# Optimization experiments

Hardware: AMD Instinct MI355X
Metric: run time of the kernel (lower is better)

Reference implementation:

```python
import jax, jax.numpy as jnp
import numpy as np

H = 16  # num heads
DH = 64  # head dim


def setup_inputs() -> dict:
    key = jax.random.key(0)
    ks = jax.random.split(key, 9)
    d = 1024
    s = 0.02
    return {
        "hidden_states": jax.random.normal(ks[0], (16, 1024, d), jnp.float32),
        "Wq": jax.random.normal(ks[1], (d, d), jnp.float32) * s,
        "bq": jax.random.normal(ks[2], (d,), jnp.float32) * s,
        "Wk": jax.random.normal(ks[3], (d, d), jnp.float32) * s,
        "bk": jax.random.normal(ks[4], (d,), jnp.float32) * s,
        "Wv": jax.random.normal(ks[5], (d, d), jnp.float32) * s,
        "bv": jax.random.normal(ks[6], (d,), jnp.float32) * s,
        "Wo": jax.random.normal(ks[7], (d, d), jnp.float32) * s,
        "bo": jax.random.normal(ks[8], (d,), jnp.float32) * s,
    }


def _heads(x):
    b, s, _ = x.shape
    return x.reshape(b, s, H, DH).transpose(0, 2, 1, 3)  # [B,H,S,Dh]


def reference(hidden_states, Wq, bq, Wk, bk, Wv, bv, Wo, bo):
    # torch nn.Linear: y = x @ W.T + b; weights here are [out, in]
    q = _heads(hidden_states @ Wq.T + bq)
    k = _heads(hidden_states @ Wk.T + bk)
    v = _heads(hidden_states @ Wv.T + bv)
    scores = jnp.einsum("bhqd,bhkd->bhqk", q, k) / jnp.sqrt(jnp.float32(DH))
    probs = jax.nn.softmax(scores, axis=-1)
    ctx = jnp.einsum("bhqk,bhkd->bhqd", probs, v)
    b, _, s, _ = ctx.shape
    ctx = ctx.transpose(0, 2, 1, 3).reshape(b, s, H * DH)
    out = ctx @ Wo.T + bo
    # module returns (attention_output, weights=None); return array only
    return out
```

## Files before the change

kernel.cpp:

```cpp
#include <hip/hip_runtime.h>
#include <hip/hip_bf16.h>
#include <stdint.h>


typedef short bf16x8 __attribute__((ext_vector_type(8)));
typedef float f32x4 __attribute__((ext_vector_type(4)));
typedef unsigned short ushort_t;
typedef ushort_t us8 __attribute__((ext_vector_type(8)));

__device__ __forceinline__ ushort_t f2b(float f) {
    unsigned x;
    __builtin_memcpy(&x, &f, 4);
    unsigned r = (x + 0x7fffu + ((x >> 16) & 1u)) >> 16;
    return (ushort_t)r;
}
__device__ __forceinline__ unsigned fbits(float f) {
    unsigned x;
    __builtin_memcpy(&x, &f, 4);
    return x;
}

__device__ __forceinline__ void glds16(const void* g, void* l) {
    __builtin_amdgcn_global_load_lds(
        (const __attribute__((address_space(1))) void*)g,
        (__attribute__((address_space(3))) void*)l, 16, 0, 0);
}

#define MFMA(a, b, c) __builtin_amdgcn_mfma_f32_16x16x32_bf16((a), (b), (c), 0, 0, 0)

__global__ __launch_bounds__(256, 8) void cvt_f32_bf16_kernel(
    const float* __restrict__ in, ushort_t* __restrict__ out, int n8)
{
    int i = blockIdx.x * 256 + threadIdx.x;
    if (i >= n8) return;
    const float4* p = (const float4*)in + (size_t)i * 2;
    float4 a = p[0], b = p[1];
    us8 v;
    v[0] = f2b(a.x); v[1] = f2b(a.y); v[2] = f2b(a.z); v[3] = f2b(a.w);
    v[4] = f2b(b.x); v[5] = f2b(b.y); v[6] = f2b(b.z); v[7] = f2b(b.w);
    *((us8*)out + i) = v;
}

template <bool OUTF>
__global__ __launch_bounds__(256, 2) void gemm_bias_kernel(
    const ushort_t* __restrict__ A,
    const ushort_t* __restrict__ W0, const ushort_t* __restrict__ W1, const ushort_t* __restrict__ W2,
    const float* __restrict__ b0, const float* __restrict__ b1, const float* __restrict__ b2,
    void* __restrict__ C0, void* __restrict__ C1, void* __restrict__ C2,
    int M, int N, int K)
{
    const ushort_t* W = (blockIdx.z == 0) ? W0 : ((blockIdx.z == 1) ? W1 : W2);
    const float* bias = (blockIdx.z == 0) ? b0 : ((blockIdx.z == 1) ? b1 : b2);
    void* C = (blockIdx.z == 0) ? C0 : ((blockIdx.z == 1) ? C1 : C2);

    __shared__ ushort_t As[128 * 64];
    __shared__ ushort_t Bs[128 * 64];

    const int tid = threadIdx.x;
    const int lane = tid & 63;
    const int wave = tid >> 6;
    const int bm = blockIdx.x * 128;
    const int bn = blockIdx.y * 128;
    const int wm = (wave >> 1) * 64;
    const int wn = (wave & 1) * 64;
    const int q = lane >> 4;
    const int ml = lane & 15;

    f32x4 acc[4][4] = {};

    for (int k0 = 0; k0 < K; k0 += 64) {
        __syncthreads();
#pragma unroll
        for (int it = 0; it < 4; ++it) {
            int cid = it * 256 + tid;
            int r = cid >> 3;
            int s = cid & 7;
            int sc = s ^ (r & 7);
            glds16(A + (size_t)(bm + r) * K + k0 + sc * 8, As + cid * 8);
            glds16(W + (size_t)(bn + r) * K + k0 + sc * 8, Bs + cid * 8);
        }
        __syncthreads();
#pragma unroll
        for (int ks = 0; ks < 2; ++ks) {
            bf16x8 af[4], bfr[4];
#pragma unroll
            for (int i = 0; i < 4; ++i) {
                int row = wm + i * 16 + ml;
                int ch = (ks * 4 + q) ^ (row & 7);
                af[i] = *(const bf16x8*)(As + row * 64 + ch * 8);
                int rowb = wn + i * 16 + ml;
                int chb = (ks * 4 + q) ^ (rowb & 7);
                bfr[i] = *(const bf16x8*)(Bs + rowb * 64 + chb * 8);
            }
#pragma unroll
            for (int i = 0; i < 4; ++i)
#pragma unroll
                for (int j = 0; j < 4; ++j)
                    acc[i][j] = MFMA(af[i], bfr[j], acc[i][j]);
        }
    }

#pragma unroll
    for (int j = 0; j < 4; ++j) {
        int col = bn + wn + j * 16 + ml;
        float bv = bias[col];
#pragma unroll
        for (int i = 0; i < 4; ++i) {
            int rowb = bm + wm + i * 16 + q * 4;
#pragma unroll
            for (int r = 0; r < 4; ++r) {
                float v = acc[i][j][r] + bv;
                if (OUTF)
                    ((float*)C)[(size_t)(rowb + r) * N + col] = v;
                else
                    ((ushort_t*)C)[(size_t)(rowb + r) * N + col] = f2b(v);
            }
        }
    }
}

__global__ __launch_bounds__(256, 4) void transpose_v_kernel(
    const ushort_t* __restrict__ V, ushort_t* __restrict__ Vt)
{
    __shared__ ushort_t t[64 * 65];
    const int bh = blockIdx.x;
    const int st = blockIdx.y;
    const int b = bh >> 4, h = bh & 15;
    const int tid = threadIdx.x;

#pragma unroll
    for (int i = 0; i < 16; ++i) {
        int e = i * 256 + tid;
        int s = e >> 6, d = e & 63;
        t[s * 65 + d] = V[(size_t)(b * 1024 + st * 64 + s) * 1024 + h * 64 + d];
    }
    __syncthreads();
#pragma unroll
    for (int i = 0; i < 16; ++i) {
        int e = i * 256 + tid;
        int d = e >> 6, s = e & 63;
        Vt[(size_t)(bh * 64 + d) * 1024 + st * 64 + s] = t[s * 65 + d];
    }
}

__global__ __launch_bounds__(256, 2) void attn_kernel(
    const ushort_t* __restrict__ Q, const ushort_t* __restrict__ K,
    const ushort_t* __restrict__ Vt, ushort_t* __restrict__ ctx)
{
    __shared__ ushort_t Ks[64 * 64];
    __shared__ ushort_t Vs[64 * 64];
    __shared__ ushort_t Ps[4][32 * 72];

    const int bh = blockIdx.x;
    const int qt = blockIdx.y;
    const int b = bh >> 4, h = bh & 15;
    const int tid = threadIdx.x;
    const int lane = tid & 63;
    const int wave = tid >> 6;
    const int q = lane >> 4;
    const int ml = lane & 15;

    bf16x8 qf[2][2];
#pragma unroll
    for (int mg = 0; mg < 2; ++mg) {
        int row = b * 1024 + qt * 128 + wave * 32 + mg * 16 + ml;
        const ushort_t* qp = Q + (size_t)row * 1024 + h * 64;
        qf[mg][0] = *(const bf16x8*)(qp + q * 8);
        qf[mg][1] = *(const bf16x8*)(qp + 32 + q * 8);
    }

    f32x4 o[2][4] = {};
    float l[2] = {0.f, 0.f};
    const float cexp = 1.4426950408889634f * 0.125f;

    ushort_t* Pw = Ps[wave];

    for (int kt = 0; kt < 16; ++kt) {
        __syncthreads();
#pragma unroll
        for (int it = 0; it < 2; ++it) {
            int cid = it * 256 + tid;
            int r = cid >> 3, s = cid & 7, sc = s ^ (r & 7);
            glds16(K + (size_t)(b * 1024 + kt * 64 + r) * 1024 + h * 64 + sc * 8,
                   Ks + cid * 8);
            glds16(Vt + (size_t)(bh * 64 + r) * 1024 + kt * 64 + sc * 8,
                   Vs + cid * 8);
        }
        __syncthreads();

#pragma unroll
        for (int n = 0; n < 4; ++n) {
            int row = n * 16 + ml;
            int c0 = q ^ (row & 7);
            int c1 = (4 + q) ^ (row & 7);
            bf16x8 k0 = *(const bf16x8*)(Ks + row * 64 + c0 * 8);
            bf16x8 k1 = *(const bf16x8*)(Ks + row * 64 + c1 * 8);
#pragma unroll
            for (int mg = 0; mg < 2; ++mg) {
                f32x4 z = {};
                z = MFMA(k0, qf[mg][0], z);
                z = MFMA(k1, qf[mg][1], z);
                float p0 = exp2f(z[0] * cexp);
                float p1 = exp2f(z[1] * cexp);
                float p2 = exp2f(z[2] * cexp);
                float p3 = exp2f(z[3] * cexp);
                l[mg] += (p0 + p1) + (p2 + p3);
                unsigned d0 = __builtin_amdgcn_perm(fbits(p1) + 0x8000u,
                                                    fbits(p0) + 0x8000u, 0x07060302u);
                unsigned d1 = __builtin_amdgcn_perm(fbits(p3) + 0x8000u,
                                                    fbits(p2) + 0x8000u, 0x07060302u);
                uint2 dd; dd.x = d0; dd.y = d1;
                *(uint2*)(Pw + (mg * 16 + ml) * 72 + n * 16 + q * 4) = dd;
            }
        }

        bf16x8 pf[2][2];
#pragma unroll
        for (int mg = 0; mg < 2; ++mg) {
            pf[mg][0] = *(const bf16x8*)(Pw + (mg * 16 + ml) * 72 + q * 8);
            pf[mg][1] = *(const bf16x8*)(Pw + (mg * 16 + ml) * 72 + 32 + q * 8);
        }

#pragma unroll
        for (int n = 0; n < 4; ++n) {
            int row = n * 16 + ml;
            int c0 = q ^ (row & 7);
            int c1 = (4 + q) ^ (row & 7);
            bf16x8 v0 = *(const bf16x8*)(Vs + row * 64 + c0 * 8);
            bf16x8 v1 = *(const bf16x8*)(Vs + row * 64 + c1 * 8);
#pragma unroll
            for (int mg = 0; mg < 2; ++mg) {
                o[mg][n] = MFMA(pf[mg][0], v0, o[mg][n]);
                o[mg][n] = MFMA(pf[mg][1], v1, o[mg][n]);
            }
        }
    }

    float li[2];
#pragma unroll
    for (int mg = 0; mg < 2; ++mg) {
        float s = l[mg];
        s += __shfl_xor(s, 16, 64);
        s += __shfl_xor(s, 32, 64);
        li[mg] = 1.0f / s;
    }

    const int orow_base = b * 1024 + qt * 128 + wave * 32;
#pragma unroll
    for (int mg = 0; mg < 2; ++mg) {
#pragma unroll
        for (int r = 0; r < 4; ++r) {
            float lv = __shfl(li[mg], q * 4 + r, 64);
            int orow = orow_base + mg * 16 + q * 4 + r;
#pragma unroll
            for (int n = 0; n < 4; ++n) {
                ctx[(size_t)orow * 1024 + h * 64 + n * 16 + ml] =
                    f2b(o[mg][n][r] * lv);
            }
        }
    }
}

extern "C" void kernel_launch(void* const* d_in, const int* in_sizes, int n_in,
                              void* d_out, int out_size, void* d_ws, size_t ws_size,
                              hipStream_t stream)
{
    const float* X  = (const float*)d_in[0];
    const float* Wq = (const float*)d_in[1];
    const float* bq = (const float*)d_in[2];
    const float* Wk = (const float*)d_in[3];
    const float* bk = (const float*)d_in[4];
    const float* Wv = (const float*)d_in[5];
    const float* bv = (const float*)d_in[6];
    const float* Wo = (const float*)d_in[7];
    const float* bo = (const float*)d_in[8];

    const int D = 1024;
    const int M = in_sizes[0] / D;
    const int Bb = M / 1024;
    const size_t MD = (size_t)M * D;
    const size_t DD = (size_t)D * D;

    ushort_t* ws  = (ushort_t*)d_ws;
    ushort_t* Xbf = ws;
    ushort_t* Qb  = ws + MD;
    ushort_t* Kb  = ws + 2 * MD;
    ushort_t* Vb  = ws + 3 * MD;
    ushort_t* Wqb = ws + 4 * MD;
    ushort_t* Wkb = Wqb + DD;
    ushort_t* Wvb = Wkb + DD;
    ushort_t* Wob = Wvb + DD;
    ushort_t* Vtb = Xbf;
    ushort_t* ctx = Vb;

    dim3 blk(256);

    cvt_f32_bf16_kernel<<<(int)(MD / 8 / 256), blk, 0, stream>>>(X, Xbf, (int)(MD / 8));
    cvt_f32_bf16_kernel<<<(int)(DD / 8 / 256), blk, 0, stream>>>(Wq, Wqb, (int)(DD / 8));
    cvt_f32_bf16_kernel<<<(int)(DD / 8 / 256), blk, 0, stream>>>(Wk, Wkb, (int)(DD / 8));
    cvt_f32_bf16_kernel<<<(int)(DD / 8 / 256), blk, 0, stream>>>(Wv, Wvb, (int)(DD / 8));
    cvt_f32_bf16_kernel<<<(int)(DD / 8 / 256), blk, 0, stream>>>(Wo, Wob, (int)(DD / 8));

    dim3 gqkv(M / 128, D / 128, 3);
    gemm_bias_kernel<false><<<gqkv, blk, 0, stream>>>(Xbf, Wqb, Wkb, Wvb, bq, bk, bv,
                                                      Qb, Kb, Vb, M, D, D);

    transpose_v_kernel<<<dim3(Bb * 16, 16), blk, 0, stream>>>(Vb, Vtb);

    attn_kernel<<<dim3(Bb * 16, 8), blk, 0, stream>>>(Qb, Kb, Vtb, ctx);

    dim3 go(M / 128, D / 128, 1);
    gemm_bias_kernel<true><<<go, blk, 0, stream>>>(ctx, Wob, Wob, Wob, bo, bo, bo,
                                                   d_out, d_out, d_out, M, D, D);
}
```

Measured before the change: 428.3 us.

## Use 32x32 MFMA in GEMM, fold softmax scale into Q, cut attention LDS

The projection GEMM switches from 16x16x32 to 32x32x16 bf16 MFMA tiles, so each wave does fewer LDS fragment loads per MFMA. The softmax scale (log2e/sqrt(dh)) is folded into the Q projection epilogue, which removes a multiply per score in attention. The attention kernel now processes one 16-row group at a time, halving the per-wave P buffer and raising launch bounds to 4 blocks per CU for occupancy. The four weight conversions are merged into one launch. Rounding Q after scaling changes numerics slightly, and the larger MFMA tile stores outputs in a strided pattern.

Measured after the change: 431.8 us. Within noise of the previous version (+0.8%).

```diff
diff --git a/kernel.cpp b/kernel.cpp
--- a/kernel.cpp
+++ b/kernel.cpp
@@ -5,6 +5,7 @@
 
 typedef short bf16x8 __attribute__((ext_vector_type(8)));
 typedef float f32x4 __attribute__((ext_vector_type(4)));
+typedef float f32x16 __attribute__((ext_vector_type(16)));
 typedef unsigned short ushort_t;
 typedef ushort_t us8 __attribute__((ext_vector_type(8)));
 
@@ -14,11 +15,6 @@
     unsigned r = (x + 0x7fffu + ((x >> 16) & 1u)) >> 16;
     return (ushort_t)r;
 }
-__device__ __forceinline__ unsigned fbits(float f) {
-    unsigned x;
-    __builtin_memcpy(&x, &f, 4);
-    return x;
-}
 
 __device__ __forceinline__ void glds16(const void* g, void* l) {
     __builtin_amdgcn_global_load_lds(
@@ -26,11 +22,19 @@
         (__attribute__((address_space(3))) void*)l, 16, 0, 0);
 }
 
-#define MFMA(a, b, c) __builtin_amdgcn_mfma_f32_16x16x32_bf16((a), (b), (c), 0, 0, 0)
-
-__global__ __launch_bounds__(256, 8) void cvt_f32_bf16_kernel(
-    const float* __restrict__ in, ushort_t* __restrict__ out, int n8)
-{
+#define MFMA16(a, b, c) __builtin_amdgcn_mfma_f32_16x16x32_bf16((a), (b), (c), 0, 0, 0)
+#define MFMA32(a, b, c) __builtin_amdgcn_mfma_f32_32x32x16_bf16((a), (b), (c), 0, 0, 0)
+
+__global__ __launch_bounds__(256, 8) void cvt4_kernel(
+    const float* __restrict__ s0, const float* __restrict__ s1,
+    const float* __restrict__ s2, const float* __restrict__ s3,
+    ushort_t* __restrict__ d0, ushort_t* __restrict__ d1,
+    ushort_t* __restrict__ d2, ushort_t* __restrict__ d3, int n8)
+{
+    const float* in = (blockIdx.y == 0) ? s0 : (blockIdx.y == 1) ? s1
+                       : (blockIdx.y == 2) ? s2 : s3;
+    ushort_t* out = (blockIdx.y == 0) ? d0 : (blockIdx.y == 1) ? d1
+                       : (blockIdx.y == 2) ? d2 : d3;
     int i = blockIdx.x * 256 + threadIdx.x;
     if (i >= n8) return;
     const float4* p = (const float4*)in + (size_t)i * 2;
@@ -41,17 +45,32 @@
     *((us8*)out + i) = v;
 }
 
+__global__ __launch_bounds__(256, 8) void cvt1_kernel(
+    const float* __restrict__ in, ushort_t* __restrict__ out, int n8)
+{
+    int i = blockIdx.x * 256 + threadIdx.x;
+    if (i >= n8) return;
+    const float4* p = (const float4*)in + (size_t)i * 2;
+    float4 a = p[0], b = p[1];
+    us8 v;
+    v[0] = f2b(a.x); v[1] = f2b(a.y); v[2] = f2b(a.z); v[3] = f2b(a.w);
+    v[4] = f2b(b.x); v[5] = f2b(b.y); v[6] = f2b(b.z); v[7] = f2b(b.w);
+    *((us8*)out + i) = v;
+}
+
 template <bool OUTF>
 __global__ __launch_bounds__(256, 2) void gemm_bias_kernel(
     const ushort_t* __restrict__ A,
     const ushort_t* __restrict__ W0, const ushort_t* __restrict__ W1, const ushort_t* __restrict__ W2,
     const float* __restrict__ b0, const float* __restrict__ b1, const float* __restrict__ b2,
     void* __restrict__ C0, void* __restrict__ C1, void* __restrict__ C2,
+    float s0, float s1, float s2,
     int M, int N, int K)
 {
     const ushort_t* W = (blockIdx.z == 0) ? W0 : ((blockIdx.z == 1) ? W1 : W2);
     const float* bias = (blockIdx.z == 0) ? b0 : ((blockIdx.z == 1) ? b1 : b2);
     void* C = (blockIdx.z == 0) ? C0 : ((blockIdx.z == 1) ? C1 : C2);
+    const float scale = (blockIdx.z == 0) ? s0 : ((blockIdx.z == 1) ? s1 : s2);
 
     __shared__ ushort_t As[128 * 64];
     __shared__ ushort_t Bs[128 * 64];
@@ -63,10 +82,10 @@
     const int bn = blockIdx.y * 128;
     const int wm = (wave >> 1) * 64;
     const int wn = (wave & 1) * 64;
-    const int q = lane >> 4;
-    const int ml = lane & 15;
-
-    f32x4 acc[4][4] = {};
+    const int r32 = lane & 31;
+    const int g = lane >> 5;
+
+    f32x16 acc[2][2] = {};
 
     for (int k0 = 0; k0 < K; k0 += 64) {
         __syncthreads();
@@ -81,39 +100,40 @@
         }
         __syncthreads();
 #pragma unroll
-        for (int ks = 0; ks < 2; ++ks) {
-            bf16x8 af[4], bfr[4];
-#pragma unroll
-            for (int i = 0; i < 4; ++i) {
-                int row = wm + i * 16 + ml;
-                int ch = (ks * 4 + q) ^ (row & 7);
+        for (int kk = 0; kk < 4; ++kk) {
+            bf16x8 af[2], bfr[2];
+#pragma unroll
+            for (int i = 0; i < 2; ++i) {
+                int row = wm + i * 32 + r32;
+                int ch = (kk * 2 + g) ^ (row & 7);
                 af[i] = *(const bf16x8*)(As + row * 64 + ch * 8);
-                int rowb = wn + i * 16 + ml;
-                int chb = (ks * 4 + q) ^ (rowb & 7);
+                int rowb = wn + i * 32 + r32;
+                int chb = (kk * 2 + g) ^ (rowb & 7);
                 bfr[i] = *(const bf16x8*)(Bs + rowb * 64 + chb * 8);
             }
 #pragma unroll
-            for (int i = 0; i < 4; ++i)
-#pragma unroll
-                for (int j = 0; j < 4; ++j)
-                    acc[i][j] = MFMA(af[i], bfr[j], acc[i][j]);
-        }
-    }
-
-#pragma unroll
-    for (int j = 0; j < 4; ++j) {
-        int col = bn + wn + j * 16 + ml;
+            for (int i = 0; i < 2; ++i)
+#pragma unroll
+                for (int j = 0; j < 2; ++j)
+                    acc[i][j] = MFMA32(af[i], bfr[j], acc[i][j]);
+        }
+    }
+
+#pragma unroll
+    for (int j = 0; j < 2; ++j) {
+        int col = bn + wn + j * 32 + r32;
         float bv = bias[col];
 #pragma unroll
-        for (int i = 0; i < 4; ++i) {
-            int rowb = bm + wm + i * 16 + q * 4;
-#pragma unroll
-            for (int r = 0; r < 4; ++r) {
-                float v = acc[i][j][r] + bv;
+        for (int i = 0; i < 2; ++i) {
+            int rbase = bm + wm + i * 32 + 4 * g;
+#pragma unroll
+            for (int reg = 0; reg < 16; ++reg) {
+                int row = rbase + (reg & 3) + 8 * (reg >> 2);
+                float v = (acc[i][j][reg] + bv) * scale;
                 if (OUTF)
-                    ((float*)C)[(size_t)(rowb + r) * N + col] = v;
+                    ((float*)C)[(size_t)row * N + col] = v;
                 else
-                    ((ushort_t*)C)[(size_t)(rowb + r) * N + col] = f2b(v);
+                    ((ushort_t*)C)[(size_t)row * N + col] = f2b(v);
             }
         }
     }
@@ -143,13 +163,13 @@
     }
 }
 
-__global__ __launch_bounds__(256, 2) void attn_kernel(
+__global__ __launch_bounds__(256, 4) void attn_kernel(
     const ushort_t* __restrict__ Q, const ushort_t* __restrict__ K,
     const ushort_t* __restrict__ Vt, ushort_t* __restrict__ ctx)
 {
     __shared__ ushort_t Ks[64 * 64];
     __shared__ ushort_t Vs[64 * 64];
-    __shared__ ushort_t Ps[4][32 * 72];
+    __shared__ ushort_t Ps[4][16 * 72];
 
     const int bh = blockIdx.x;
     const int qt = blockIdx.y;
@@ -171,8 +191,6 @@
 
     f32x4 o[2][4] = {};
     float l[2] = {0.f, 0.f};
-    const float cexp = 1.4426950408889634f * 0.125f;
-
     ushort_t* Pw = Ps[wave];
 
     for (int kt = 0; kt < 16; ++kt) {
@@ -189,49 +207,42 @@
         __syncthreads();
 
 #pragma unroll
-        for (int n = 0; n < 4; ++n) {
-            int row = n * 16 + ml;
-            int c0 = q ^ (row & 7);
-            int c1 = (4 + q) ^ (row & 7);
-            bf16x8 k0 = *(const bf16x8*)(Ks + row * 64 + c0 * 8);
-            bf16x8 k1 = *(const bf16x8*)(Ks + row * 64 + c1 * 8);
-#pragma unroll
-            for (int mg = 0; mg < 2; ++mg) {
+        for (int mg = 0; mg < 2; ++mg) {
+#pragma unroll
+            for (int n = 0; n < 4; ++n) {
+                int row = n * 16 + ml;
+                int c0 = q ^ (row & 7);
+                int c1 = (4 + q) ^ (row & 7);
+                bf16x8 k0 = *(const bf16x8*)(Ks + row * 64 + c0 * 8);
+                bf16x8 k1 = *(const bf16x8*)(Ks + row * 64 + c1 * 8);
                 f32x4 z = {};
-                z = MFMA(k0, qf[mg][0], z);
-                z = MFMA(k1, qf[mg][1], z);
-                float p0 = exp2f(z[0] * cexp);
-                float p1 = exp2f(z[1] * cexp);
-                float p2 = exp2f(z[2] * cexp);
-                float p3 = exp2f(z[3] * cexp);
+                z = MFMA16(k0, qf[mg][0], z);
+                z = MFMA16(k1, qf[mg][1], z);
+                float p0 = exp2f(z[0]);
+                float p1 = exp2f(z[1]);
+                float p2 = exp2f(z[2]);
+                float p3 = exp2f(z[3]);
                 l[mg] += (p0 + p1) + (p2 + p3);
-                unsigned d0 = __builtin_amdgcn_perm(fbits(p1) + 0x8000u,
-                                                    fbits(p0) + 0x8000u, 0x07060302u);
-                unsigned d1 = __builtin_amdgcn_perm(fbits(p3) + 0x8000u,
-                                                    fbits(p2) + 0x8000u, 0x07060302u);
-                uint2 dd; dd.x = d0; dd.y = d1;
-                *(uint2*)(Pw + (mg * 16 + ml) * 72 + n * 16 + q * 4) = dd;
-            }
-        }
-
-        bf16x8 pf[2][2];
-#pragma unroll
-        for (int mg = 0; mg < 2; ++mg) {
-            pf[mg][0] = *(const bf16x8*)(Pw + (mg * 16 + ml) * 72 + q * 8);
-            pf[mg][1] = *(const bf16x8*)(Pw + (mg * 16 + ml) * 72 + 32 + q * 8);
-        }
-
-#pragma unroll
-        for (int n = 0; n < 4; ++n) {
-            int row = n * 16 + ml;
-            int c0 = q ^ (row & 7);
-            int c1 = (4 + q) ^ (row & 7);
-            bf16x8 v0 = *(const bf16x8*)(Vs + row * 64 + c0 * 8);
-            bf16x8 v1 = *(const bf16x8*)(Vs + row * 64 + c1 * 8);
-#pragma unroll
-            for (int mg = 0; mg < 2; ++mg) {
-                o[mg][n] = MFMA(pf[mg][0], v0, o[mg][n]);
-                o[mg][n] = MFMA(pf[mg][1], v1, o[mg][n]);
+                __hip_bfloat162 h01 = __float22bfloat162_rn(make_float2(p0, p1));
+                __hip_bfloat162 h23 = __float22bfloat162_rn(make_float2(p2, p3));
+                uint2 dd;
+                __builtin_memcpy(&dd.x, &h01, 4);
+                __builtin_memcpy(&dd.y, &h23, 4);
+                *(uint2*)(Pw + ml * 72 + n * 16 + q * 4) = dd;
+            }
+
+            bf16x8 pf0 = *(const bf16x8*)(Pw + ml * 72 + q * 8);
+            bf16x8 pf1 = *(const bf16x8*)(Pw + ml * 72 + 32 + q * 8);
+
+#pragma unroll
+            for (int n = 0; n < 4; ++n) {
+                int row = n * 16 + ml;
+                int c0 = q ^ (row & 7);
+                int c1 = (4 + q) ^ (row & 7);
+                bf16x8 v0 = *(const bf16x8*)(Vs + row * 64 + c0 * 8);
+                bf16x8 v1 = *(const bf16x8*)(Vs + row * 64 + c1 * 8);
+                o[mg][n] = MFMA16(pf0, v0, o[mg][n]);
+                o[mg][n] = MFMA16(pf1, v1, o[mg][n]);
             }
         }
     }
@@ -295,15 +306,15 @@
 
     dim3 blk(256);
 
-    cvt_f32_bf16_kernel<<<(int)(MD / 8 / 256), blk, 0, stream>>>(X, Xbf, (int)(MD / 8));
-    cvt_f32_bf16_kernel<<<(int)(DD / 8 / 256), blk, 0, stream>>>(Wq, Wqb, (int)(DD / 8));
-    cvt_f32_bf16_kernel<<<(int)(DD / 8 / 256), blk, 0, stream>>>(Wk, Wkb, (int)(DD / 8));
-    cvt_f32_bf16_kernel<<<(int)(DD / 8 / 256), blk, 0, stream>>>(Wv, Wvb, (int)(DD / 8));
-    cvt_f32_bf16_kernel<<<(int)(DD / 8 / 256), blk, 0, stream>>>(Wo, Wob, (int)(DD / 8));
-
+    cvt1_kernel<<<(int)(MD / 8 / 256), blk, 0, stream>>>(X, Xbf, (int)(MD / 8));
+    cvt4_kernel<<<dim3((int)(DD / 8 / 256), 4), blk, 0, stream>>>(
+        Wq, Wk, Wv, Wo, Wqb, Wkb, Wvb, Wob, (int)(DD / 8));
+
+    const float qscale = 1.4426950408889634f * 0.125f;
     dim3 gqkv(M / 128, D / 128, 3);
     gemm_bias_kernel<false><<<gqkv, blk, 0, stream>>>(Xbf, Wqb, Wkb, Wvb, bq, bk, bv,
-                                                      Qb, Kb, Vb, M, D, D);
+                                                      Qb, Kb, Vb,
+                                                      qscale, 1.0f, 1.0f, M, D, D);
 
     transpose_v_kernel<<<dim3(Bb * 16, 16), blk, 0, stream>>>(Vb, Vtb);
 
@@ -311,5 +322,6 @@
 
     dim3 go(M / 128, D / 128, 1);
     gemm_bias_kernel<true><<<go, blk, 0, stream>>>(ctx, Wob, Wob, Wob, bo, bo, bo,
-                                                   d_out, d_out, d_out, M, D, D);
-}
+                                                   d_out, d_out, d_out,
+                                                   1.0f, 1.0f, 1.0f, M, D, D);
+}
```
